# Kernel optimization log

Measured on AMD Instinct MI355X. Metric: run time of the kernel, lower is better.

## Reference

```python
import jax, jax.numpy as jnp
import numpy as np

B, S, I, O = 64, 64, 64, 64   # batch, seq, input bits, output bits
N, M, H = 1024, 64, 256       # memory addresses, content bits, controller hidden
EPS = 1e-8


def setup_inputs() -> dict:
    key = jax.random.key(0)
    ks = jax.random.split(key, 6)
    sc = 0.05
    P = 4 * M + 12  # read head: M+6 params, write head: M+6 addressing + M erase + M add
    return {
        "inputs_BxSxI": jax.random.normal(ks[0], (B, S, I), jnp.float32),
        "Wx": (jax.random.normal(ks[1], (I + M, 4 * H)) * sc).astype(jnp.float32),
        "Wh": (jax.random.normal(ks[2], (H, 4 * H)) * sc).astype(jnp.float32),
        "b_lstm": jnp.zeros((4 * H,), jnp.float32),
        "W_head": (jax.random.normal(ks[3], (H, P)) * sc).astype(jnp.float32),
        "b_head": jnp.zeros((P,), jnp.float32),
        "W_out": (jax.random.normal(ks[4], (H + M, O)) * sc).astype(jnp.float32),
        "b_out": jnp.zeros((O,), jnp.float32),
    }


def _address(k, beta, g, s, gamma, w_prev, mem):
    """NTM addressing: content (cosine) -> interpolate -> circular shift -> sharpen."""
    dot = jnp.einsum('bm,bnm->bn', k, mem)                                  # [B,N]
    sim = dot / (jnp.linalg.norm(k, axis=-1, keepdims=True)
                 * jnp.linalg.norm(mem, axis=-1) + EPS)
    wc = jax.nn.softmax(beta[:, None] * sim, axis=-1)
    wg = g[:, None] * wc + (1.0 - g[:, None]) * w_prev
    # 3-tap circular convolution with shift weights s = [shift -1, 0, +1]
    ws = s[:, 0:1] * jnp.roll(wg, -1, axis=1) + s[:, 1:2] * wg + s[:, 2:3] * jnp.roll(wg, 1, axis=1)
    wp = ws ** gamma[:, None]
    return wp / (jnp.sum(wp, axis=-1, keepdims=True) + EPS)


def _parse_head(q):
    k = jnp.tanh(q[:, :M])
    beta = jax.nn.softplus(q[:, M])
    g = jax.nn.sigmoid(q[:, M + 1])
    s = jax.nn.softmax(q[:, M + 2:M + 5], axis=-1)
    gamma = 1.0 + jax.nn.softplus(q[:, M + 5])
    return k, beta, g, s, gamma


def reference(inputs_BxSxI, Wx, Wh, b_lstm, W_head, b_head, W_out, b_out):
    Bn = inputs_BxSxI.shape[0]
    dt = inputs_BxSxI.dtype
    mem0 = jnp.full((Bn, N, M), 0.01, dt)
    w0 = jnp.zeros((Bn, N), dt).at[:, 0].set(1.0)
    h0 = jnp.zeros((Bn, H), dt)
    c0 = jnp.zeros((Bn, H), dt)
    r0 = jnp.zeros((Bn, M), dt)

    def step(carry, x_t):
        h, c, mem, w_r, w_w, r = carry
        # LSTM controller on [input; prev read vector]
        gates = jnp.concatenate([x_t, r], -1) @ Wx + h @ Wh + b_lstm
        i_g, f_g, g_g, o_g = jnp.split(gates, 4, axis=-1)
        c = jax.nn.sigmoid(f_g) * c + jax.nn.sigmoid(i_g) * jnp.tanh(g_g)
        h = jax.nn.sigmoid(o_g) * jnp.tanh(c)
        # interface parameters
        p = h @ W_head + b_head
        pr, pw = p[:, :M + 6], p[:, M + 6:]
        w_r = _address(*_parse_head(pr), w_r, mem)
        w_w = _address(*_parse_head(pw[:, :M + 6]), w_w, mem)
        e = jax.nn.sigmoid(pw[:, M + 6:2 * M + 6])   # erase vector [B,M]
        a = pw[:, 2 * M + 6:]                        # add vector   [B,M]
        # read from (pre-write) memory, then erase/add write
        r = jnp.einsum('bn,bnm->bm', w_r, mem)
        mem = mem * (1.0 - w_w[:, :, None] * e[:, None, :]) + w_w[:, :, None] * a[:, None, :]
        out = jnp.concatenate([h, r], -1) @ W_out + b_out
        return (h, c, mem, w_r, w_w, r), out

    _, outs = jax.lax.scan(step, (h0, c0, mem0, w0, w0, r0), jnp.swapaxes(inputs_BxSxI, 0, 1))
    return jnp.swapaxes(outs, 0, 1)  # [B,S,O]
```

## Files before the change

### kernel.cpp

```cpp
#include <hip/hip_runtime.h>
#include <math.h>

#define B_  64
#define S_  64
#define I_  64
#define O_  64
#define N_  1024
#define M_  64
#define H_  256
#define G4  1024
#define P_  268
#define EPSF 1e-8f

__device__ __forceinline__ float sigmoidf_(float x){ return 1.0f/(1.0f+expf(-x)); }
__device__ __forceinline__ float softplusf_(float x){ return fmaxf(x,0.0f)+log1pf(expf(-fabsf(x))); }

__device__ __forceinline__ float2 block_sum2(float2 v, float2* redbuf){
  int tid=threadIdx.x, lane=tid&63, wid=tid>>6;
  #pragma unroll
  for(int t=32;t;t>>=1){ v.x+=__shfl_xor(v.x,t,64); v.y+=__shfl_xor(v.y,t,64); }
  if(lane==0) redbuf[wid]=v;
  __syncthreads();
  float2 a=redbuf[0];
  #pragma unroll
  for(int i=1;i<16;i++){ float2 t2=redbuf[i]; a.x+=t2.x; a.y+=t2.y; }
  __syncthreads();
  return a;
}

__device__ __forceinline__ float2 block_max2(float2 v, float2* redbuf){
  int tid=threadIdx.x, lane=tid&63, wid=tid>>6;
  #pragma unroll
  for(int t=32;t;t>>=1){ v.x=fmaxf(v.x,__shfl_xor(v.x,t,64)); v.y=fmaxf(v.y,__shfl_xor(v.y,t,64)); }
  if(lane==0) redbuf[wid]=v;
  __syncthreads();
  float2 a=redbuf[0];
  #pragma unroll
  for(int i=1;i<16;i++){ float2 t2=redbuf[i]; a.x=fmaxf(a.x,t2.x); a.y=fmaxf(a.y,t2.y); }
  __syncthreads();
  return a;
}

extern "C" __global__ __launch_bounds__(1024)
void ntm_persistent(const float* __restrict__ X,
                    const float* __restrict__ Wx,
                    const float* __restrict__ Wh,
                    const float* __restrict__ bl,
                    const float* __restrict__ Whd,
                    const float* __restrict__ bh,
                    const float* __restrict__ Wo,
                    const float* __restrict__ bo,
                    float* __restrict__ out,
                    float* __restrict__ ws_mem)
{
  const int b    = blockIdx.x;
  const int tid  = threadIdx.x;
  const int lane = tid & 63;
  const int wid  = tid >> 6;

  __shared__ float h_s[H_], c_s[H_], r_s[M_], xr[I_+M_];
  __shared__ float gates[G4];
  __shared__ float p_s[P_];
  __shared__ float k_r[M_], k_w[M_], e_s[M_], a_s[M_];
  __shared__ float w_r[N_], w_w[N_];
  __shared__ float wg_r[N_], wg_w[N_];
  __shared__ float part[16][M_];
  __shared__ float2 redbuf[16];
  __shared__ float sc_beta_r, sc_g_r, sc_s_r0, sc_s_r1, sc_s_r2, sc_gamma_r;
  __shared__ float sc_beta_w, sc_g_w, sc_s_w0, sc_s_w1, sc_s_w2, sc_gamma_w;
  __shared__ float nk_r, nk_w;

  float* mem = ws_mem + (size_t)b * (N_*M_);

  for(int i=tid;i<N_*M_;i+=1024) mem[i] = 0.01f;
  if(tid<H_){ h_s[tid]=0.f; c_s[tid]=0.f; }
  if(tid<M_) r_s[tid]=0.f;
  w_r[tid] = (tid==0)?1.f:0.f;
  w_w[tid] = (tid==0)?1.f:0.f;
  __syncthreads();

  for(int s=0;s<S_;s++){
    if(tid<I_)            xr[tid] = X[((size_t)b*S_+s)*I_+tid];
    else if(tid<I_+M_)    xr[tid] = r_s[tid-I_];
    __syncthreads();

    {
      float acc = bl[tid];
      #pragma unroll 4
      for(int i=0;i<I_+M_;i++) acc += xr[i]*Wx[i*G4+tid];
      #pragma unroll 4
      for(int k=0;k<H_;k++)    acc += h_s[k]*Wh[k*G4+tid];
      gates[tid]=acc;
    }
    __syncthreads();

    if(tid<H_){
      float ig=gates[tid], fg=gates[256+tid], gg=gates[512+tid], og=gates[768+tid];
      float cn = sigmoidf_(fg)*c_s[tid] + sigmoidf_(ig)*tanhf(gg);
      c_s[tid]=cn;
      h_s[tid]=sigmoidf_(og)*tanhf(cn);
    }
    __syncthreads();

    if(tid<P_){
      float acc = bh[tid];
      #pragma unroll 4
      for(int k=0;k<H_;k++) acc += h_s[k]*Whd[k*P_+tid];
      p_s[tid]=acc;
    }
    __syncthreads();

    if(wid==0){
      float kv = tanhf(p_s[lane]); k_r[lane]=kv;
      float sq = kv*kv;
      #pragma unroll
      for(int t=32;t;t>>=1) sq += __shfl_xor(sq,t,64);
      if(lane==0) nk_r = sqrtf(sq);
    } else if(wid==1){
      float kv = tanhf(p_s[70+lane]); k_w[lane]=kv;
      float sq = kv*kv;
      #pragma unroll
      for(int t=32;t;t>>=1) sq += __shfl_xor(sq,t,64);
      if(lane==0) nk_w = sqrtf(sq);
    } else if(wid==2){
      e_s[lane] = sigmoidf_(p_s[140+lane]);
    } else if(wid==3){
      a_s[lane] = p_s[204+lane];
    } else if(tid==256){
      sc_beta_r = softplusf_(p_s[64]);
      sc_g_r    = sigmoidf_(p_s[65]);
      float m3=fmaxf(p_s[66],fmaxf(p_s[67],p_s[68]));
      float e0=expf(p_s[66]-m3), e1=expf(p_s[67]-m3), e2=expf(p_s[68]-m3);
      float ss=e0+e1+e2;
      sc_s_r0=e0/ss; sc_s_r1=e1/ss; sc_s_r2=e2/ss;
      sc_gamma_r = 1.0f+softplusf_(p_s[69]);
    } else if(tid==320){
      sc_beta_w = softplusf_(p_s[134]);
      sc_g_w    = sigmoidf_(p_s[135]);
      float m3=fmaxf(p_s[136],fmaxf(p_s[137],p_s[138]));
      float e0=expf(p_s[136]-m3), e1=expf(p_s[137]-m3), e2=expf(p_s[138]-m3);
      float ss=e0+e1+e2;
      sc_s_w0=e0/ss; sc_s_w1=e1/ss; sc_s_w2=e2/ss;
      sc_gamma_w = 1.0f+softplusf_(p_s[139]);
    }
    __syncthreads();

    float dot_r=0.f, dot_w=0.f, nsq=0.f;
    {
      const float* row = mem + (size_t)tid*M_;
      #pragma unroll 4
      for(int m=0;m<M_;m+=4){
        float4 v = *reinterpret_cast<const float4*>(row+m);
        dot_r += v.x*k_r[m]   + v.y*k_r[m+1] + v.z*k_r[m+2] + v.w*k_r[m+3];
        dot_w += v.x*k_w[m]   + v.y*k_w[m+1] + v.z*k_w[m+2] + v.w*k_w[m+3];
        nsq   += v.x*v.x + v.y*v.y + v.z*v.z + v.w*v.w;
      }
    }
    float nmem = sqrtf(nsq);
    float sim_r = dot_r/(nk_r*nmem+EPSF);
    float sim_w = dot_w/(nk_w*nmem+EPSF);
    float scr = sc_beta_r*sim_r, scw = sc_beta_w*sim_w;
    float2 mx = block_max2(make_float2(scr,scw), redbuf);
    float er = expf(scr-mx.x), ew = expf(scw-mx.y);
    float2 sm = block_sum2(make_float2(er,ew), redbuf);
    float wc_r = er/sm.x, wc_w = ew/sm.y;

    float wgr = sc_g_r*wc_r + (1.f-sc_g_r)*w_r[tid];
    float wgw = sc_g_w*wc_w + (1.f-sc_g_w)*w_w[tid];
    wg_r[tid]=wgr; wg_w[tid]=wgw;
    __syncthreads();

    int np1=(tid+1)&(N_-1), nm1=(tid+N_-1)&(N_-1);
    float wsr = sc_s_r0*wg_r[np1] + sc_s_r1*wgr + sc_s_r2*wg_r[nm1];
    float wsw = sc_s_w0*wg_w[np1] + sc_s_w1*wgw + sc_s_w2*wg_w[nm1];
    float wpr = powf(wsr, sc_gamma_r);
    float wpw = powf(wsw, sc_gamma_w);
    float2 sp = block_sum2(make_float2(wpr,wpw), redbuf);
    float wnr = wpr/(sp.x+EPSF), wnw = wpw/(sp.y+EPSF);
    w_r[tid]=wnr; w_w[tid]=wnw;
    __syncthreads();

    float racc = 0.f;
    {
      const float em = e_s[lane], am = a_s[lane];
      #pragma unroll 4
      for(int nn=0;nn<64;nn++){
        int n = (wid<<6)+nn;
        float wrn = w_r[n], wwn = w_w[n];
        float v = mem[(size_t)n*M_+lane];
        racc += wrn*v;
        mem[(size_t)n*M_+lane] = v*(1.f - wwn*em) + wwn*am;
      }
    }
    part[wid][lane]=racc;
    __syncthreads();
    if(tid<M_){
      float acc=0.f;
      #pragma unroll
      for(int g2=0;g2<16;g2++) acc+=part[g2][tid];
      r_s[tid]=acc;
    }
    __syncthreads();

    {
      float acc=0.f;
      int k0=wid*20;
      #pragma unroll
      for(int kk=0;kk<20;kk++){
        int k=k0+kk;
        float hv = (k<H_)? h_s[k] : r_s[k-H_];
        acc += hv*Wo[k*O_+lane];
      }
      part[wid][lane]=acc;
    }
    __syncthreads();
    if(tid<O_){
      float acc=bo[tid];
      #pragma unroll
      for(int g2=0;g2<16;g2++) acc+=part[g2][tid];
      out[((size_t)b*S_+s)*O_+tid]=acc;
    }
    __syncthreads();
  }
}

extern "C" void kernel_launch(void* const* d_in, const int* in_sizes, int n_in,
                              void* d_out, int out_size, void* d_ws, size_t ws_size,
                              hipStream_t stream)
{
  const float* X   = (const float*)d_in[0];
  const float* Wx  = (const float*)d_in[1];
  const float* Wh  = (const float*)d_in[2];
  const float* bl  = (const float*)d_in[3];
  const float* Whd = (const float*)d_in[4];
  const float* bh  = (const float*)d_in[5];
  const float* Wo  = (const float*)d_in[6];
  const float* bo  = (const float*)d_in[7];
  float* out = (float*)d_out;
  float* mem = (float*)d_ws;

  hipLaunchKernelGGL(ntm_persistent, dim3(B_), dim3(1024), 0, stream,
                     X, Wx, Wh, bl, Whd, bh, Wo, bo, out, mem);
}
```

Baseline: 2.964 ms.

## Transpose memory layout to column-major, split gate GEMV across halves, parallelize head projection

Stores the per-batch NTM memory as [M][N] instead of [N][M], so the content-similarity pass reads coalesced columns per address and the read/erase-add pass has each wave handle four content columns with a shuffle reduction instead of a shared-memory partial sum. The LSTM gate GEMV is split by K across the two halves of the block, each thread computing two adjacent columns via float2 loads, with partial sums stored in the reused wg_r/wg_w buffers. The head projection is spread across all 16 waves with a K-split and a shared-memory reduction, rather than using only 268 threads. The goal is better coalescing and more active threads per step, at the cost of extra shared memory and an extra barrier.

```diff
diff --git a/kernel.cpp b/kernel.cpp
--- a/kernel.cpp
+++ b/kernel.cpp
@@ -58,13 +58,13 @@
   const int lane = tid & 63;
   const int wid  = tid >> 6;
 
-  __shared__ float h_s[H_], c_s[H_], r_s[M_], xr[I_+M_];
-  __shared__ float gates[G4];
+  __shared__ float h_s[H_], c_s[H_], r_s[M_], xr[128];
   __shared__ float p_s[P_];
   __shared__ float k_r[M_], k_w[M_], e_s[M_], a_s[M_];
   __shared__ float w_r[N_], w_w[N_];
   __shared__ float wg_r[N_], wg_w[N_];
   __shared__ float part[16][M_];
+  __shared__ float part2[16][272];
   __shared__ float2 redbuf[16];
   __shared__ float sc_beta_r, sc_g_r, sc_s_r0, sc_s_r1, sc_s_r2, sc_gamma_r;
   __shared__ float sc_beta_w, sc_g_w, sc_s_w0, sc_s_w1, sc_s_w2, sc_gamma_w;
@@ -79,33 +79,72 @@
   w_w[tid] = (tid==0)?1.f:0.f;
   __syncthreads();
 
+  const int half = tid >> 9;
+  const int tc   = tid & 511;
+
   for(int s=0;s<S_;s++){
-    if(tid<I_)            xr[tid] = X[((size_t)b*S_+s)*I_+tid];
-    else if(tid<I_+M_)    xr[tid] = r_s[tid-I_];
-    __syncthreads();
-
-    {
-      float acc = bl[tid];
-      #pragma unroll 4
-      for(int i=0;i<I_+M_;i++) acc += xr[i]*Wx[i*G4+tid];
-      #pragma unroll 4
-      for(int k=0;k<H_;k++)    acc += h_s[k]*Wh[k*G4+tid];
-      gates[tid]=acc;
+    if(tid<I_)        xr[tid] = X[((size_t)b*S_+s)*I_+tid];
+    else if(tid<128)  xr[tid] = r_s[tid-I_];
+    __syncthreads();
+
+    {
+      float g0=0.f, g1=0.f;
+      const int c0 = 2*tc;
+      if(half==0){
+        #pragma unroll 8
+        for(int k=0;k<128;k++){
+          float2 w = *reinterpret_cast<const float2*>(Wx + (size_t)k*G4 + c0);
+          float x = xr[k];
+          g0 += x*w.x; g1 += x*w.y;
+        }
+        #pragma unroll 8
+        for(int k=0;k<64;k++){
+          float2 w = *reinterpret_cast<const float2*>(Wh + (size_t)k*G4 + c0);
+          float x = h_s[k];
+          g0 += x*w.x; g1 += x*w.y;
+        }
+        wg_r[c0]=g0; wg_r[c0+1]=g1;
+      } else {
+        #pragma unroll 8
+        for(int k=64;k<256;k++){
+          float2 w = *reinterpret_cast<const float2*>(Wh + (size_t)k*G4 + c0);
+          float x = h_s[k];
+          g0 += x*w.x; g1 += x*w.y;
+        }
+        wg_w[c0]=g0; wg_w[c0+1]=g1;
+      }
     }
     __syncthreads();
 
     if(tid<H_){
-      float ig=gates[tid], fg=gates[256+tid], gg=gates[512+tid], og=gates[768+tid];
+      float ig = wg_r[tid]      + wg_w[tid]      + bl[tid];
+      float fg = wg_r[256+tid]  + wg_w[256+tid]  + bl[256+tid];
+      float gg = wg_r[512+tid]  + wg_w[512+tid]  + bl[512+tid];
+      float og = wg_r[768+tid]  + wg_w[768+tid]  + bl[768+tid];
       float cn = sigmoidf_(fg)*c_s[tid] + sigmoidf_(ig)*tanhf(gg);
       c_s[tid]=cn;
       h_s[tid]=sigmoidf_(og)*tanhf(cn);
     }
     __syncthreads();
 
+    {
+      const int k0 = wid*16;
+      #pragma unroll
+      for(int p=0;p<5;p++){
+        int c = p*64 + lane;
+        if(c<P_){
+          float acc=0.f;
+          #pragma unroll
+          for(int kk=0;kk<16;kk++) acc += h_s[k0+kk]*Whd[(size_t)(k0+kk)*P_ + c];
+          part2[wid][c]=acc;
+        }
+      }
+    }
+    __syncthreads();
     if(tid<P_){
       float acc = bh[tid];
-      #pragma unroll 4
-      for(int k=0;k<H_;k++) acc += h_s[k]*Whd[k*P_+tid];
+      #pragma unroll
+      for(int g2=0;g2<16;g2++) acc += part2[g2][tid];
       p_s[tid]=acc;
     }
     __syncthreads();
@@ -147,13 +186,10 @@
 
     float dot_r=0.f, dot_w=0.f, nsq=0.f;
     {
-      const float* row = mem + (size_t)tid*M_;
-      #pragma unroll 4
-      for(int m=0;m<M_;m+=4){
-        float4 v = *reinterpret_cast<const float4*>(row+m);
-        dot_r += v.x*k_r[m]   + v.y*k_r[m+1] + v.z*k_r[m+2] + v.w*k_r[m+3];
-        dot_w += v.x*k_w[m]   + v.y*k_w[m+1] + v.z*k_w[m+2] + v.w*k_w[m+3];
-        nsq   += v.x*v.x + v.y*v.y + v.z*v.z + v.w*v.w;
+      #pragma unroll 8
+      for(int m=0;m<M_;m++){
+        float v = mem[(size_t)m*N_ + tid];
+        dot_r += v*k_r[m]; dot_w += v*k_w[m]; nsq += v*v;
       }
     }
     float nmem = sqrtf(nsq);
@@ -180,25 +216,32 @@
     w_r[tid]=wnr; w_w[tid]=wnw;
     __syncthreads();
 
-    float racc = 0.f;
-    {
-      const float em = e_s[lane], am = a_s[lane];
+    {
+      float racc0=0.f,racc1=0.f,racc2=0.f,racc3=0.f;
+      const int m0 = wid*4;
+      const float em0=e_s[m0], em1=e_s[m0+1], em2=e_s[m0+2], em3=e_s[m0+3];
+      const float am0=a_s[m0], am1=a_s[m0+1], am2=a_s[m0+2], am3=a_s[m0+3];
+      float* c0p = mem + (size_t)m0*N_;
       #pragma unroll 4
-      for(int nn=0;nn<64;nn++){
-        int n = (wid<<6)+nn;
+      for(int t=0;t<16;t++){
+        int n = t*64 + lane;
         float wrn = w_r[n], wwn = w_w[n];
-        float v = mem[(size_t)n*M_+lane];
-        racc += wrn*v;
-        mem[(size_t)n*M_+lane] = v*(1.f - wwn*em) + wwn*am;
-      }
-    }
-    part[wid][lane]=racc;
-    __syncthreads();
-    if(tid<M_){
-      float acc=0.f;
-      #pragma unroll
-      for(int g2=0;g2<16;g2++) acc+=part[g2][tid];
-      r_s[tid]=acc;
+        float v0 = c0p[n];
+        float v1 = c0p[N_+n];
+        float v2 = c0p[2*N_+n];
+        float v3 = c0p[3*N_+n];
+        racc0 += wrn*v0; racc1 += wrn*v1; racc2 += wrn*v2; racc3 += wrn*v3;
+        c0p[n]       = v0*(1.f - wwn*em0) + wwn*am0;
+        c0p[N_+n]    = v1*(1.f - wwn*em1) + wwn*am1;
+        c0p[2*N_+n]  = v2*(1.f - wwn*em2) + wwn*am2;
+        c0p[3*N_+n]  = v3*(1.f - wwn*em3) + wwn*am3;
+      }
+      #pragma unroll
+      for(int t=32;t;t>>=1){
+        racc0+=__shfl_xor(racc0,t,64); racc1+=__shfl_xor(racc1,t,64);
+        racc2+=__shfl_xor(racc2,t,64); racc3+=__shfl_xor(racc3,t,64);
+      }
+      if(lane==0){ r_s[m0]=racc0; r_s[m0+1]=racc1; r_s[m0+2]=racc2; r_s[m0+3]=racc3; }
     }
     __syncthreads();
 
@@ -209,7 +252,7 @@
       for(int kk=0;kk<20;kk++){
         int k=k0+kk;
         float hv = (k<H_)? h_s[k] : r_s[k-H_];
-        acc += hv*Wo[k*O_+lane];
+        acc += hv*Wo[(size_t)k*O_+lane];
       }
       part[wid][lane]=acc;
     }
```

New measurement: 6.201 ms. +109.2%, slower.
